# Optimization experiments

Hardware: AMD Instinct MI355X
Metric: run time of the kernel (lower is better)

The kernel has to match this reference:

```python
import jax, jax.numpy as jnp
import numpy as np

B, NC, NP, K, C, DIN, TS, M = 4, 1024, 32768, 3, 256, 448, 2, 4
EPS = 1e-5


def _mlp3(x, w0, b0, w1, b1, w2, b2):
    x = jax.nn.relu(x @ w0 + b0)
    x = jax.nn.relu(x @ w1 + b1)
    return x @ w2 + b2


def setup_inputs():
    key = jax.random.key(0)
    ks = jax.random.split(key, 32)
    f = lambda i, shape, s=0.02: jax.random.normal(ks[i], shape, jnp.float32) * s
    iw = jax.random.uniform(ks[0], (B, NP, K), jnp.float32)
    iw = iw / iw.sum(-1, keepdims=True)  # KNN interpolation weights sum to 1
    return {
        'pc_embeddings': f(1, (B, NC, DIN), 1.0),
        'pc_pe': f(2, (B, NC, C), 1.0),
        'sparse_prompt': f(3, (B, TS, C), 1.0),
        'dense_prompt': f(4, (B, NC, C), 1.0),
        'pf_feat': f(5, (B, NP, DIN), 1.0),
        'interp_weight': iw,
        'interp_index': jax.random.randint(ks[6], (B, NP, K), 0, NC),
        'iou_token': f(7, (1, C)),
        'mask_tokens': f(8, (M, C)),
        'enc_w0': f(9, (DIN, C)), 'enc_b0': jnp.zeros((C,), jnp.float32),
        'enc_w1': f(10, (C, C)), 'enc_b1': jnp.zeros((C,), jnp.float32),
        'enc_w2': f(11, (C, C)), 'enc_b2': jnp.zeros((C,), jnp.float32),
        'up_w0': f(12, (C + DIN, C)), 'up_b0': jnp.zeros((C,), jnp.float32),
        'ln_g': jnp.ones((C,), jnp.float32), 'ln_b': jnp.zeros((C,), jnp.float32),
        'up_w1': f(13, (C, C)), 'up_b1': jnp.zeros((C,), jnp.float32),
        'hyp_w0': f(14, (M, C, C)), 'hyp_b0': jnp.zeros((M, C), jnp.float32),
        'hyp_w1': f(15, (M, C, C)), 'hyp_b1': jnp.zeros((M, C), jnp.float32),
        'hyp_w2': f(16, (M, C, C)), 'hyp_b2': jnp.zeros((M, C), jnp.float32),
        'iou_w0': f(17, (C, 256)), 'iou_b0': jnp.zeros((256,), jnp.float32),
        'iou_w1': f(18, (256, 256)), 'iou_b1': jnp.zeros((256,), jnp.float32),
        'iou_w2': f(19, (256, M)), 'iou_b2': jnp.zeros((M,), jnp.float32),
    }


def reference(pc_embeddings, pc_pe, sparse_prompt, dense_prompt, pf_feat,
              interp_weight, interp_index, iou_token, mask_tokens,
              enc_w0, enc_b0, enc_w1, enc_b1, enc_w2, enc_b2,
              up_w0, up_b0, ln_g, ln_b, up_w1, up_b1,
              hyp_w0, hyp_b0, hyp_w1, hyp_b1, hyp_w2, hyp_b2,
              iou_w0, iou_b0, iou_w1, iou_b1, iou_w2, iou_b2):
    # encoder_mapper: MLP 448 -> 256 (relu between layers)
    pc_emb = _mlp3(pc_embeddings, enc_w0, enc_b0, enc_w1, enc_b1, enc_w2, enc_b2)
    out_tok = jnp.concatenate([iou_token, mask_tokens], 0)  # [1+M, C]
    tokens = jnp.concatenate(
        [jnp.broadcast_to(out_tok[None], (B, 1 + M, C)), sparse_prompt], 1)
    src = pc_emb + dense_prompt  # [B, NC, C]
    # transformer stand-in (identity): hs = tokens, src unchanged; pc_pe unused
    hs = tokens
    iou_token_out = hs[:, 0]            # [B, C]
    mask_tokens_out = hs[:, 1:1 + M]    # [B, M, C]
    # interpolate_features: irregular gather of k=3 neighbor center embeddings
    idx = interp_index.astype(jnp.int32).reshape(B, NP * K, 1)
    gathered = jnp.take_along_axis(src, idx, axis=1).reshape(B, NP, K, C)
    interp = (gathered * interp_weight[..., None]).sum(2)  # [B, NP, C]
    x = jnp.concatenate([interp, pf_feat], -1)  # [B, NP, C+448]
    # output_upscaling: Linear -> LayerNorm -> GELU -> Linear -> GELU
    x = x @ up_w0 + up_b0
    mu = x.mean(-1, keepdims=True)
    var = ((x - mu) ** 2).mean(-1, keepdims=True)
    x = (x - mu) * jax.lax.rsqrt(var + EPS) * ln_g + ln_b
    x = jax.nn.gelu(x, approximate=False)
    upscaled = jax.nn.gelu(x @ up_w1 + up_b1, approximate=False)  # [B, NP, C]
    # per-mask-token hypernetwork MLPs (batched over the M tokens)
    h = jax.nn.relu(jnp.einsum('bmc,mcd->bmd', mask_tokens_out, hyp_w0) + hyp_b0[None])
    h = jax.nn.relu(jnp.einsum('bmc,mcd->bmd', h, hyp_w1) + hyp_b1[None])
    hyper = jnp.einsum('bmc,mcd->bmd', h, hyp_w2) + hyp_b2[None]
    hyper = hyper[:, 1:]  # multimask_output=True -> slice(1, None)
    masks = jnp.einsum('bmc,bnc->bmn', hyper, upscaled)  # [B, M-1, NP]
    iou_pred = _mlp3(iou_token_out, iou_w0, iou_b0, iou_w1, iou_b1, iou_w2, iou_b2)[:, 1:]
    return masks, iou_pred
```

## Files before the change

### kernel.cpp

```cpp
#include <hip/hip_runtime.h>
#include <hip/hip_bf16.h>
#include <math.h>

constexpr int kB   = 4;
constexpr int kNC  = 1024;
constexpr int kNP  = 32768;
constexpr int kC   = 256;
constexpr int kDIN = 448;
constexpr int kM   = 4;

typedef __attribute__((ext_vector_type(8))) short short8;
typedef __attribute__((ext_vector_type(4))) float float4v;
typedef __attribute__((ext_vector_type(4))) unsigned short ushort4v;

__device__ __forceinline__ float gelu_exact(float x) {
    return 0.5f * x * (1.0f + erff(x * 0.70710678118654752440f));
}
__device__ __forceinline__ unsigned short f2bf(float f) {
    unsigned int u = __float_as_uint(f);
    unsigned int r = (u + 0x7fffu + ((u >> 16) & 1u)) >> 16;
    return (unsigned short)r;
}
__device__ __forceinline__ float bf2f(unsigned short s) {
    return __uint_as_float(((unsigned int)s) << 16);
}
__device__ __forceinline__ unsigned int pk_bf16(float lo, float hi) {
    __hip_bfloat162 h = __float22bfloat162_rn(float2{lo, hi});
    union { __hip_bfloat162 h; unsigned int u; } c;
    c.h = h;
    return c.u;
}

__global__ __launch_bounds__(256) void prep_weights(
    const float* __restrict__ ew0, const float* __restrict__ ew1,
    const float* __restrict__ ew2, const float* __restrict__ uw0,
    const float* __restrict__ uw1,
    unsigned short* __restrict__ ew0s, unsigned short* __restrict__ ew1s,
    unsigned short* __restrict__ ew2s, unsigned short* __restrict__ w0as,
    unsigned short* __restrict__ w0bs, unsigned short* __restrict__ w1s_)
{
    const int bx = blockIdx.x, t = threadIdx.x;
    const float* srcW; int k0; unsigned short* dst;
    if (bx < 14)      { srcW = ew0; k0 = bx * 32;              dst = ew0s + bx * 8192; }
    else if (bx < 22) { srcW = ew1; k0 = (bx - 14) * 32;       dst = ew1s + (bx - 14) * 8192; }
    else if (bx < 30) { srcW = ew2; k0 = (bx - 22) * 32;       dst = ew2s + (bx - 22) * 8192; }
    else if (bx < 38) { srcW = uw0; k0 = (bx - 30) * 32;       dst = w0as + (bx - 30) * 8192; }
    else if (bx < 52) { srcW = uw0; k0 = 256 + (bx - 38) * 32; dst = w0bs + (bx - 38) * 8192; }
    else              { srcW = uw1; k0 = (bx - 52) * 32;       dst = w1s_ + (bx - 52) * 8192; }
    unsigned short v[32];
    #pragma unroll
    for (int kk = 0; kk < 32; ++kk) v[kk] = f2bf(srcW[(size_t)(k0 + kk) * kC + t]);
    #pragma unroll
    for (int j = 0; j < 4; ++j) *(short8*)(dst + t * 32 + j * 8) = *(short8*)(v + j * 8);
}

__device__ __forceinline__ void gemm_x2_global(
    const unsigned short* __restrict__ x2e, const unsigned short* __restrict__ wsrc,
    int nchunk, int w, int q, int ml, float4v acc[4][4])
{
    const unsigned short* wp[4];
    #pragma unroll
    for (int ct = 0; ct < 4; ++ct) wp[ct] = wsrc + ((64 * w + 16 * ct + ml) * 32 + q * 8);
    for (int c = 0; c < nchunk; ++c) {
        short8 af[4], bfr[4];
        #pragma unroll
        for (int rt = 0; rt < 4; ++rt)
            af[rt] = *(const short8*)(x2e + (16 * rt + ml) * 264 + c * 32 + q * 8);
        #pragma unroll
        for (int ct = 0; ct < 4; ++ct) bfr[ct] = *(const short8*)(wp[ct] + c * 8192);
        #pragma unroll
        for (int rt = 0; rt < 4; ++rt)
            #pragma unroll
            for (int ct = 0; ct < 4; ++ct)
                acc[rt][ct] = __builtin_amdgcn_mfma_f32_16x16x32_bf16(af[rt], bfr[ct], acc[rt][ct], 0, 0, 0);
    }
}

__device__ __forceinline__ void gemm_x1_global(
    const unsigned short* __restrict__ x2e, const unsigned short* __restrict__ wsrc,
    int nchunk, int w, int q, int ml, float4v acc[4])
{
    const unsigned short* wp[4];
    #pragma unroll
    for (int ct = 0; ct < 4; ++ct) wp[ct] = wsrc + ((64 * w + 16 * ct + ml) * 32 + q * 8);
    for (int c = 0; c < nchunk; ++c) {
        short8 af = *(const short8*)(x2e + ml * 264 + c * 32 + q * 8);
        short8 bfr[4];
        #pragma unroll
        for (int ct = 0; ct < 4; ++ct) bfr[ct] = *(const short8*)(wp[ct] + c * 8192);
        #pragma unroll
        for (int ct = 0; ct < 4; ++ct)
            acc[ct] = __builtin_amdgcn_mfma_f32_16x16x32_bf16(af, bfr[ct], acc[ct], 0, 0, 0);
    }
}

__global__ __launch_bounds__(256) void kernelA(
    const float* __restrict__ pc, const float* __restrict__ dense,
    const unsigned short* __restrict__ ew0s, const float* __restrict__ eb0,
    const unsigned short* __restrict__ ew1s, const float* __restrict__ eb1,
    const unsigned short* __restrict__ ew2s, const float* __restrict__ eb2,
    const unsigned short* __restrict__ w0as, const float* __restrict__ ub0,
    const float* __restrict__ iou_token, const float* __restrict__ mask_tokens,
    const float* __restrict__ hw0, const float* __restrict__ hb0,
    const float* __restrict__ hw1, const float* __restrict__ hb1,
    const float* __restrict__ hw2, const float* __restrict__ hb2,
    const float* __restrict__ iw0, const float* __restrict__ ib0,
    const float* __restrict__ iw1, const float* __restrict__ ib1,
    const float* __restrict__ iw2, const float* __restrict__ ib2,
    unsigned short* __restrict__ Zbf,
    float* __restrict__ hyper_out,
    float* __restrict__ iou_out)
{
    __shared__ unsigned short x2e[16 * 264];
    __shared__ float va[kC];
    __shared__ float vb[kC];
    const int tid = threadIdx.x, bx = blockIdx.x;

    if (bx >= 5) {
        const int row0 = (bx - 5) * 16;
        const int w = tid >> 6, lane = tid & 63, q = lane >> 4, ml = lane & 15;

        const float* pcr = pc + (size_t)(row0 + ml) * kDIN;
        float4v acc0[4] = {};
        for (int c = 0; c < 14; ++c) {
            float4 f0 = *(const float4*)(pcr + c * 32 + q * 8);
            float4 f1 = *(const float4*)(pcr + c * 32 + q * 8 + 4);
            union { short8 s; unsigned int u[4]; } cv;
            cv.u[0] = pk_bf16(f0.x, f0.y); cv.u[1] = pk_bf16(f0.z, f0.w);
            cv.u[2] = pk_bf16(f1.x, f1.y); cv.u[3] = pk_bf16(f1.z, f1.w);
            short8 af = cv.s;
            #pragma unroll
            for (int ct = 0; ct < 4; ++ct) {
                short8 bfr = *(const short8*)(ew0s + (size_t)c * 8192 + (64 * w + 16 * ct + ml) * 32 + q * 8);
                acc0[ct] = __builtin_amdgcn_mfma_f32_16x16x32_bf16(af, bfr, acc0[ct], 0, 0, 0);
            }
        }
        {
            float bc[4];
            #pragma unroll
            for (int ct = 0; ct < 4; ++ct) bc[ct] = eb0[64 * w + 16 * ct + ml];
            #pragma unroll
            for (int i = 0; i < 4; ++i) {
                int row = 4 * q + i;
                #pragma unroll
                for (int ct = 0; ct < 4; ++ct)
                    x2e[row * 264 + 64 * w + 16 * ct + ml] = f2bf(fmaxf(acc0[ct][i] + bc[ct], 0.0f));
            }
        }
        __syncthreads();

        float4v acc2[4] = {};
        gemm_x1_global(x2e, ew1s, 8, w, q, ml, acc2);
        __syncthreads();
        {
            float bc[4];
            #pragma unroll
            for (int ct = 0; ct < 4; ++ct) bc[ct] = eb1[64 * w + 16 * ct + ml];
            #pragma unroll
            for (int i = 0; i < 4; ++i) {
                int row = 4 * q + i;
                #pragma unroll
                for (int ct = 0; ct < 4; ++ct)
                    x2e[row * 264 + 64 * w + 16 * ct + ml] = f2bf(fmaxf(acc2[ct][i] + bc[ct], 0.0f));
            }
        }
        __syncthreads();

        float4v acc3[4] = {};
        gemm_x1_global(x2e, ew2s, 8, w, q, ml, acc3);
        __syncthreads();
        {
            float bc[4];
            #pragma unroll
            for (int ct = 0; ct < 4; ++ct) bc[ct] = eb2[64 * w + 16 * ct + ml];
            #pragma unroll
            for (int i = 0; i < 4; ++i) {
                int row = 4 * q + i;
                #pragma unroll
                for (int ct = 0; ct < 4; ++ct) {
                    int col = 64 * w + 16 * ct + ml;
                    float v = acc3[ct][i] + bc[ct] + dense[(size_t)(row0 + row) * kC + col];
                    x2e[row * 264 + col] = f2bf(v);
                }
            }
        }
        __syncthreads();

        float4v accZ[4] = {};
        gemm_x1_global(x2e, w0as, 8, w, q, ml, accZ);
        {
            float bc[4];
            #pragma unroll
            for (int ct = 0; ct < 4; ++ct) bc[ct] = ub0[64 * w + 16 * ct + ml];
            #pragma unroll
            for (int i = 0; i < 4; ++i) {
                int row = 4 * q + i;
                ushort4v o;
                #pragma unroll
                for (int ct = 0; ct < 4; ++ct) o[ct] = f2bf(accZ[ct][i] + bc[ct]);
                *(ushort4v*)(Zbf + (size_t)(row0 + row) * kC + 64 * w + 4 * ml) = o;
            }
        }
    } else if (bx < 4) {
        const int m = bx;
        va[tid] = mask_tokens[m * kC + tid];
        __syncthreads();
        const float* W = hw0 + (size_t)m * kC * kC;
        float acc = hb0[m * kC + tid];
        for (int d = 0; d < kC; d++) acc = fmaf(va[d], W[d * kC + tid], acc);
        vb[tid] = fmaxf(acc, 0.0f);
        __syncthreads();
        W = hw1 + (size_t)m * kC * kC;
        acc = hb1[m * kC + tid];
        for (int d = 0; d < kC; d++) acc = fmaf(vb[d], W[d * kC + tid], acc);
        va[tid] = fmaxf(acc, 0.0f);
        __syncthreads();
        W = hw2 + (size_t)m * kC * kC;
        acc = hb2[m * kC + tid];
        for (int d = 0; d < kC; d++) acc = fmaf(va[d], W[d * kC + tid], acc);
        if (m >= 1) hyper_out[(m - 1) * kC + tid] = acc;
    } else {
        va[tid] = iou_token[tid];
        __syncthreads();
        float acc = ib0[tid];
        for (int d = 0; d < kC; d++) acc = fmaf(va[d], iw0[d * 256 + tid], acc);
        vb[tid] = fmaxf(acc, 0.0f);
        __syncthreads();
        acc = ib1[tid];
        for (int d = 0; d < 256; d++) acc = fmaf(vb[d], iw1[d * 256 + tid], acc);
        va[tid] = fmaxf(acc, 0.0f);
        __syncthreads();
        if (tid < kM) {
            acc = ib2[tid];
            for (int d = 0; d < 256; d++) acc = fmaf(va[d], iw2[d * kM + tid], acc);
            if (tid >= 1)
                for (int b = 0; b < kB; b++) iou_out[b * 3 + (tid - 1)] = acc;
        }
    }
}

__global__ __launch_bounds__(256, 3) void main_mfma(
    const unsigned short* __restrict__ Zbf,
    const float* __restrict__ pf,
    const float* __restrict__ iwgt, const int* __restrict__ iidx,
    const unsigned short* __restrict__ w0bs, const unsigned short* __restrict__ w1s_,
    const float* __restrict__ lng, const float* __restrict__ lnb,
    const float* __restrict__ b1v, const float* __restrict__ hyper,
    float* __restrict__ masks)
{
    __shared__ unsigned short x2[64 * 264];
    __shared__ int   gi[64][3];
    __shared__ float gw[64][3];
    __shared__ float sums[4][64];
    __shared__ float sqs[4][64];
    __shared__ float muA[64];
    __shared__ float rsA[64];
    __shared__ float pd[12][64];

    const int b = blockIdx.y, p0 = blockIdx.x * 64, tid = threadIdx.x;
    const int w = tid >> 6, lane = tid & 63, q = lane >> 4, ml = lane & 15;

    if (tid < 192) {
        int r = tid / 3, k = tid - r * 3;
        int base = (b * kNP + p0 + r) * 3 + k;
        gi[r][k] = iidx[base];
        gw[r][k] = iwgt[base];
    }
    __syncthreads();

    const float* pfr[4];
    #pragma unroll
    for (int rt = 0; rt < 4; ++rt)
        pfr[rt] = pf + ((size_t)b * kNP + p0 + 16 * rt + ml) * kDIN;
    const unsigned short* wbp[4];
    #pragma unroll
    for (int ct = 0; ct < 4; ++ct) wbp[ct] = w0bs + ((64 * w + 16 * ct + ml) * 32 + q * 8);

    float4v acc[4][4] = {};
    for (int c = 0; c < 14; ++c) {
        short8 af[4], bfr[4];
        #pragma unroll
        for (int rt = 0; rt < 4; ++rt) {
            float4 f0 = *(const float4*)(pfr[rt] + c * 32 + q * 8);
            float4 f1 = *(const float4*)(pfr[rt] + c * 32 + q * 8 + 4);
            union { short8 s; unsigned int u[4]; } cv;
            cv.u[0] = pk_bf16(f0.x, f0.y); cv.u[1] = pk_bf16(f0.z, f0.w);
            cv.u[2] = pk_bf16(f1.x, f1.y); cv.u[3] = pk_bf16(f1.z, f1.w);
            af[rt] = cv.s;
        }
        #pragma unroll
        for (int ct = 0; ct < 4; ++ct) bfr[ct] = *(const short8*)(wbp[ct] + c * 8192);
        #pragma unroll
        for (int rt = 0; rt < 4; ++rt)
            #pragma unroll
            for (int ct = 0; ct < 4; ++ct)
                acc[rt][ct] = __builtin_amdgcn_mfma_f32_16x16x32_bf16(af[rt], bfr[ct], acc[rt][ct], 0, 0, 0);
    }

    {
        const unsigned short* zb = Zbf + (size_t)b * kNC * kC + 64 * w + 4 * ml;
        #pragma unroll
        for (int rt = 0; rt < 4; ++rt)
            #pragma unroll
            for (int i = 0; i < 4; ++i) {
                int row = 16 * rt + 4 * q + i;
                #pragma unroll
                for (int k = 0; k < 3; ++k) {
                    float wk = gw[row][k];
                    ushort4v z = *(const ushort4v*)(zb + (size_t)gi[row][k] * kC);
                    #pragma unroll
                    for (int ct = 0; ct < 4; ++ct)
                        acc[rt][ct][i] = fmaf(wk, bf2f(z[ct]), acc[rt][ct][i]);
                }
            }
    }

    {
        float s[4][4], s2[4][4];
        #pragma unroll
        for (int rt = 0; rt < 4; ++rt)
            #pragma unroll
            for (int i = 0; i < 4; ++i) {
                float a = 0.f, b2 = 0.f;
                #pragma unroll
                for (int ct = 0; ct < 4; ++ct) {
                    float v = acc[rt][ct][i];
                    a += v; b2 = fmaf(v, v, b2);
                }
                s[rt][i] = a; s2[rt][i] = b2;
            }
        #pragma unroll
        for (int o = 1; o < 16; o <<= 1) {
            #pragma unroll
            for (int rt = 0; rt < 4; ++rt)
                #pragma unroll
                for (int i = 0; i < 4; ++i) {
                    s[rt][i]  += __shfl_xor(s[rt][i], o);
                    s2[rt][i] += __shfl_xor(s2[rt][i], o);
                }
        }
        if (ml == 0) {
            #pragma unroll
            for (int rt = 0; rt < 4; ++rt)
                #pragma unroll
                for (int i = 0; i < 4; ++i) {
                    int row = 16 * rt + 4 * q + i;
                    sums[w][row] = s[rt][i];
                    sqs[w][row]  = s2[rt][i];
                }
        }
    }
    __syncthreads();
    if (tid < 64) {
        float ts = sums[0][tid] + sums[1][tid] + sums[2][tid] + sums[3][tid];
        float tq = sqs[0][tid] + sqs[1][tid] + sqs[2][tid] + sqs[3][tid];
        float mu = ts * (1.0f / 256.0f);
        float var = tq * (1.0f / 256.0f) - mu * mu;
        muA[tid] = mu;
        rsA[tid] = rsqrtf(var + 1e-5f);
    }
    __syncthreads();

    {
        float gc[4], oc[4];
        #pragma unroll
        for (int ct = 0; ct < 4; ++ct) {
            gc[ct] = lng[64 * w + 16 * ct + ml];
            oc[ct] = lnb[64 * w + 16 * ct + ml];
        }
        #pragma unroll
        for (int rt = 0; rt < 4; ++rt)
            #pragma unroll
            for (int i = 0; i < 4; ++i) {
                int row = 16 * rt + 4 * q + i;
                float mu = muA[row], rs = rsA[row];
                #pragma unroll
                for (int ct = 0; ct < 4; ++ct) {
                    float v = (acc[rt][ct][i] - mu) * rs * gc[ct] + oc[ct];
                    x2[row * 264 + 64 * w + 16 * ct + ml] = f2bf(gelu_exact(v));
                }
            }
    }
    __syncthreads();

    float4v acc2[4][4] = {};
    gemm_x2_global(x2, w1s_, 8, w, q, ml, acc2);

    {
        float bc1[4], hy[3][4];
        #pragma unroll
        for (int ct = 0; ct < 4; ++ct) bc1[ct] = b1v[64 * w + 16 * ct + ml];
        #pragma unroll
        for (int m = 0; m < 3; ++m)
            #pragma unroll
            for (int ct = 0; ct < 4; ++ct) hy[m][ct] = hyper[m * kC + 64 * w + 16 * ct + ml];
        float pdl[3][4][4] = {};
        #pragma unroll
        for (int rt = 0; rt < 4; ++rt)
            #pragma unroll
            for (int ct = 0; ct < 4; ++ct)
                #pragma unroll
                for (int i = 0; i < 4; ++i) {
                    float u = gelu_exact(acc2[rt][ct][i] + bc1[ct]);
                    #pragma unroll
                    for (int m = 0; m < 3; ++m) pdl[m][rt][i] = fmaf(u, hy[m][ct], pdl[m][rt][i]);
                }
        #pragma unroll
        for (int o = 1; o < 16; o <<= 1) {
            #pragma unroll
            for (int m = 0; m < 3; ++m)
                #pragma unroll
                for (int rt = 0; rt < 4; ++rt)
                    #pragma unroll
                    for (int i = 0; i < 4; ++i)
                        pdl[m][rt][i] += __shfl_xor(pdl[m][rt][i], o);
        }
        if (ml < 3) {
            const int m = ml;
            #pragma unroll
            for (int rt = 0; rt < 4; ++rt)
                #pragma unroll
                for (int i = 0; i < 4; ++i)
                    pd[w * 3 + m][16 * rt + 4 * q + i] = pdl[m][rt][i];
        }
    }
    __syncthreads();
    if (tid < 192) {
        int m = tid >> 6, r = tid & 63;
        float v = pd[0 + m][r] + pd[3 + m][r] + pd[6 + m][r] + pd[9 + m][r];
        masks[((size_t)b * 3 + m) * kNP + p0 + r] = v;
    }
}

extern "C" void kernel_launch(void* const* d_in, const int* in_sizes, int n_in,
                              void* d_out, int out_size, void* d_ws, size_t ws_size,
                              hipStream_t stream) {
    const float* pc_emb  = (const float*)d_in[0];
    const float* dense   = (const float*)d_in[3];
    const float* pf      = (const float*)d_in[4];
    const float* iwgt    = (const float*)d_in[5];
    const int*   iidx    = (const int*)d_in[6];
    const float* iou_tok = (const float*)d_in[7];
    const float* mtok    = (const float*)d_in[8];
    const float* ew0 = (const float*)d_in[9];
    const float* eb0 = (const float*)d_in[10];
    const float* ew1 = (const float*)d_in[11];
    const float* eb1 = (const float*)d_in[12];
    const float* ew2 = (const float*)d_in[13];
    const float* eb2 = (const float*)d_in[14];
    const float* uw0 = (const float*)d_in[15];
    const float* ub0 = (const float*)d_in[16];
    const float* lng = (const float*)d_in[17];
    const float* lnb = (const float*)d_in[18];
    const float* uw1 = (const float*)d_in[19];
    const float* ub1 = (const float*)d_in[20];
    const float* hw0 = (const float*)d_in[21];
    const float* hb0 = (const float*)d_in[22];
    const float* hw1 = (const float*)d_in[23];
    const float* hb1 = (const float*)d_in[24];
    const float* hw2 = (const float*)d_in[25];
    const float* hb2 = (const float*)d_in[26];
    const float* iw0 = (const float*)d_in[27];
    const float* ib0 = (const float*)d_in[28];
    const float* iw1 = (const float*)d_in[29];
    const float* ib1 = (const float*)d_in[30];
    const float* iw2 = (const float*)d_in[31];
    const float* ib2 = (const float*)d_in[32];

    float* out = (float*)d_out;

    char* ws = (char*)d_ws;
    unsigned short* Zbf  = (unsigned short*)(ws + 0);
    float* ws_hyper      = (float*)(ws + 2097152);
    unsigned short* ew0s = (unsigned short*)(ws + 2100224);
    unsigned short* ew1s = (unsigned short*)(ws + 2329600);
    unsigned short* ew2s = (unsigned short*)(ws + 2460672);
    unsigned short* w0as = (unsigned short*)(ws + 2591744);
    unsigned short* w0bs = (unsigned short*)(ws + 2722816);
    unsigned short* w1s_ = (unsigned short*)(ws + 2952192);

    prep_weights<<<60, 256, 0, stream>>>(ew0, ew1, ew2, uw0, uw1,
                                         ew0s, ew1s, ew2s, w0as, w0bs, w1s_);

    kernelA<<<261, 256, 0, stream>>>(
        pc_emb, dense, ew0s, eb0, ew1s, eb1, ew2s, eb2, w0as, ub0,
        iou_tok, mtok, hw0, hb0, hw1, hb1, hw2, hb2,
        iw0, ib0, iw1, ib1, iw2, ib2,
        Zbf, ws_hyper, out + (size_t)kB * 3 * kNP);

    main_mfma<<<dim3(kNP / 64, kB), 256, 0, stream>>>(
        Zbf, pf, iwgt, iidx, w0bs, w1s_,
        lng, lnb, ub1, ws_hyper, out);
}
```

Baseline: 637.9 us.

## Stage pf_feat tile through shared memory once per block instead of per-wave reloads

The first GEMM previously had each of the 4 waves load and convert the same 64x448 fp32 pf_feat rows straight from global memory, so every row was fetched four times. The block now loads the tile cooperatively in two halves of 224 columns, converts it to bf16 into a shared buffer (reusing the x2 LDS array), and the MFMA A fragments are read from LDS. This removes redundant global traffic and conversions. In exchange it adds two barriers per half and LDS read traffic, and loses the overlap between global loads and MFMAs within a wave.

New measurement: 615.7 us. -3.5%, faster.

```diff
diff --git a/kernel.cpp b/kernel.cpp
--- a/kernel.cpp
+++ b/kernel.cpp
@@ -248,7 +248,7 @@
     const float* __restrict__ b1v, const float* __restrict__ hyper,
     float* __restrict__ masks)
 {
-    __shared__ unsigned short x2[64 * 264];
+    __shared__ unsigned short buf[64 * 264];
     __shared__ int   gi[64][3];
     __shared__ float gw[64][3];
     __shared__ float sums[4][64];
@@ -266,35 +266,42 @@
         gi[r][k] = iidx[base];
         gw[r][k] = iwgt[base];
     }
-    __syncthreads();
-
-    const float* pfr[4];
+
+    float4v acc[4][4] = {};
+    const float* pfb = pf + ((size_t)b * kNP + p0) * kDIN;
+
     #pragma unroll
-    for (int rt = 0; rt < 4; ++rt)
-        pfr[rt] = pf + ((size_t)b * kNP + p0 + 16 * rt + ml) * kDIN;
-    const unsigned short* wbp[4];
-    #pragma unroll
-    for (int ct = 0; ct < 4; ++ct) wbp[ct] = w0bs + ((64 * w + 16 * ct + ml) * 32 + q * 8);
-
-    float4v acc[4][4] = {};
-    for (int c = 0; c < 14; ++c) {
-        short8 af[4], bfr[4];
-        #pragma unroll
-        for (int rt = 0; rt < 4; ++rt) {
-            float4 f0 = *(const float4*)(pfr[rt] + c * 32 + q * 8);
-            float4 f1 = *(const float4*)(pfr[rt] + c * 32 + q * 8 + 4);
+    for (int h = 0; h < 2; ++h) {
+        #pragma unroll
+        for (int j = 0; j < 7; ++j) {
+            int idx = j * 256 + tid;
+            int r = idx / 28;
+            int co = idx - r * 28;
+            const float* g = pfb + (size_t)r * kDIN + h * 224 + co * 8;
+            float4 f0 = *(const float4*)g;
+            float4 f1 = *(const float4*)(g + 4);
             union { short8 s; unsigned int u[4]; } cv;
             cv.u[0] = pk_bf16(f0.x, f0.y); cv.u[1] = pk_bf16(f0.z, f0.w);
             cv.u[2] = pk_bf16(f1.x, f1.y); cv.u[3] = pk_bf16(f1.z, f1.w);
-            af[rt] = cv.s;
-        }
-        #pragma unroll
-        for (int ct = 0; ct < 4; ++ct) bfr[ct] = *(const short8*)(wbp[ct] + c * 8192);
-        #pragma unroll
-        for (int rt = 0; rt < 4; ++rt)
+            *(short8*)&buf[r * 232 + co * 8] = cv.s;
+        }
+        __syncthreads();
+        const unsigned short* wh = w0bs + (size_t)h * 7 * 8192 + ((64 * w + ml) * 32 + q * 8);
+        for (int c = 0; c < 7; ++c) {
+            short8 af[4], bfr[4];
+            #pragma unroll
+            for (int rt = 0; rt < 4; ++rt)
+                af[rt] = *(const short8*)&buf[(16 * rt + ml) * 232 + c * 32 + q * 8];
             #pragma unroll
             for (int ct = 0; ct < 4; ++ct)
-                acc[rt][ct] = __builtin_amdgcn_mfma_f32_16x16x32_bf16(af[rt], bfr[ct], acc[rt][ct], 0, 0, 0);
+                bfr[ct] = *(const short8*)(wh + (size_t)c * 8192 + 512 * ct);
+            #pragma unroll
+            for (int rt = 0; rt < 4; ++rt)
+                #pragma unroll
+                for (int ct = 0; ct < 4; ++ct)
+                    acc[rt][ct] = __builtin_amdgcn_mfma_f32_16x16x32_bf16(af[rt], bfr[ct], acc[rt][ct], 0, 0, 0);
+        }
+        __syncthreads();
     }
 
     {
@@ -377,14 +384,14 @@
                 #pragma unroll
                 for (int ct = 0; ct < 4; ++ct) {
                     float v = (acc[rt][ct][i] - mu) * rs * gc[ct] + oc[ct];
-                    x2[row * 264 + 64 * w + 16 * ct + ml] = f2bf(gelu_exact(v));
+                    buf[row * 264 + 64 * w + 16 * ct + ml] = f2bf(gelu_exact(v));
                 }
             }
     }
     __syncthreads();
 
     float4v acc2[4][4] = {};
-    gemm_x2_global(x2, w1s_, 8, w, q, ml, acc2);
+    gemm_x2_global(buf, w1s_, 8, w, q, ml, acc2);
 
     {
         float bc1[4], hy[3][4];
```
